# Optimization experiments

Measured on AMD Instinct MI355X. Metric: run time of the kernel, lower is better.

The kernel has to match this reference:

```python
import jax, jax.numpy as jnp
import numpy as np

HEADS = 8
DIM_HEAD = 64
WINDOW = 512
SCALE = DIM_HEAD ** -0.5


def setup_inputs() -> dict:
    key = jax.random.key(0)
    k1, k2, k3 = jax.random.split(key, 3)
    b, dim, n = 2, 256, 32768
    hidden = HEADS * DIM_HEAD  # 512
    x = jax.random.normal(k1, (b, dim, n), dtype=jnp.float32)
    # Conv1d(dim, hidden*3, 1, bias=False) weight -> [3*hidden, dim]
    w_qkv = jax.random.normal(k2, (3 * hidden, dim), dtype=jnp.float32) * (dim ** -0.5)
    # Conv1d(hidden, dim, 1) weight/bias
    w_out = jax.random.normal(k3, (dim, hidden), dtype=jnp.float32) * (hidden ** -0.5)
    b_out = jnp.zeros((dim,), dtype=jnp.float32)
    return {"x": x, "w_qkv": w_qkv, "w_out": w_out, "b_out": b_out}


def reference(x, w_qkv, w_out, b_out):
    b, c, n = x.shape
    h, d, w = HEADS, DIM_HEAD, WINDOW
    nw = n // w  # n chosen divisible by window size
    # 1x1 conv == channel matmul
    qkv = jnp.einsum('oc,bcn->bon', w_qkv, x)  # [b, 3*h*d, n]
    q, k, v = jnp.split(qkv, 3, axis=1)
    # [b, h, d, nw, w]
    def to_windows(t):
        return t.reshape(b, h, d, nw, w)
    q = to_windows(q) * SCALE
    k = to_windows(k)
    v = to_windows(v)
    # non-overlapping local windows: block-diagonal attention
    sim = jnp.einsum('bhdni,bhdnj->bhnij', q, k)        # [b,h,nw,w,w]
    attn = jax.nn.softmax(sim, axis=-1)
    out = jnp.einsum('bhnij,bhdnj->bhdni', attn, v)      # [b,h,d,nw,w]
    out = out.reshape(b, h * d, n)
    return jnp.einsum('oc,bcn->bon', w_out, out) + b_out[None, :, None]
```

## Files before the change

kernel.cpp:

```cpp
#include <hip/hip_runtime.h>
#include <stdint.h>
#include <stddef.h>


typedef _Float16 f16;
typedef _Float16 half8 __attribute__((ext_vector_type(8)));
typedef float f32x4 __attribute__((ext_vector_type(4)));

#define NSEQ 32768
#define NTOT 65536
#define WIN  512

__device__ __forceinline__ void async_copy16(const f16* g, f16* l) {
  __builtin_amdgcn_global_load_lds(
      (const __attribute__((address_space(1))) void*)g,
      (__attribute__((address_space(3))) void*)l, 16, 0, 0);
}

__device__ __forceinline__ int packrtz(float a, float b) {
  typedef __fp16 fp16v2 __attribute__((ext_vector_type(2)));
  fp16v2 h = __builtin_amdgcn_cvt_pkrtz(a, b);
  return __builtin_bit_cast(int, h);
}

__global__ __launch_bounds__(256) void convert_w(
    const float* __restrict__ wqkv, const float* __restrict__ wout,
    f16* __restrict__ wqh, f16* __restrict__ woh) {
  int idx = blockIdx.x * 256 + threadIdx.x;
  if (idx < 1536 * 256) {
    float v = wqkv[idx];
    if (idx < 512 * 256) v *= 0.18033688011112042f;
    wqh[idx] = (f16)v;
  } else {
    int j = idx - 1536 * 256;
    if (j < 256 * 512) woh[j] = (f16)wout[j];
  }
}

__global__ __launch_bounds__(256) void transpose_x(
    const float* __restrict__ x, f16* __restrict__ xT) {
  __shared__ alignas(16) float tile[32][33];
  const int tx = threadIdx.x & 31, ty = threadIdx.x >> 5;
  const int bx = blockIdx.x, by = blockIdx.y;
  const float* xb = x + (size_t)blockIdx.z * 256 * NSEQ;
  f16* xTb = xT + (size_t)blockIdx.z * NSEQ * 256;
#pragma unroll
  for (int r = 0; r < 4; ++r) {
    int c = by * 32 + ty + r * 8;
    int n = bx * 32 + tx;
    tile[ty + r * 8][tx] = xb[(size_t)c * NSEQ + n];
  }
  __syncthreads();
#pragma unroll
  for (int r = 0; r < 4; ++r) {
    int n = bx * 32 + ty + r * 8;
    int c = by * 32 + tx;
    xTb[(size_t)n * 256 + c] = (f16)tile[tx][ty + r * 8];
  }
}

template <int MODE>
__global__ __launch_bounds__(256) void gemm_k(
    const f16* __restrict__ A, const f16* __restrict__ Bm,
    void* __restrict__ outp, const float* __restrict__ bias, int K,
    int bstride, int ostride) {
  __shared__ alignas(16) f16 As[8192];
  __shared__ alignas(16) f16 Bs[8192];
  const int tid = threadIdx.x;
  const int lane = tid & 63, wid = tid >> 6;
  const int quad = lane >> 4, lid = lane & 15;
  const int row0 = blockIdx.y * 128, col0 = blockIdx.x * 128;
  const int wm = (wid >> 1) * 64, wn = (wid & 1) * 64;

  f32x4 acc[4][4];
  const f32x4 zero = {0.f, 0.f, 0.f, 0.f};
#pragma unroll
  for (int i = 0; i < 4; ++i)
#pragma unroll
    for (int j = 0; j < 4; ++j) acc[i][j] = zero;

  const int kIters = K >> 6;
  for (int kt = 0; kt < kIters; ++kt) {
    __syncthreads();
    const int k0 = kt * 64;
#pragma unroll
    for (int rd = 0; rd < 4; ++rd) {
      int slot = rd * 256 + tid;
      int r = slot & 127, kc = slot >> 7;
      async_copy16(A + (size_t)(row0 + r) * K + k0 + kc * 8, As + slot * 8);
      async_copy16(Bm + (size_t)(col0 + r) * bstride + k0 + kc * 8,
                   Bs + slot * 8);
    }
    __syncthreads();

    half8 af[2][4], bf[2][4];
#pragma unroll
    for (int ks = 0; ks < 2; ++ks) {
#pragma unroll
      for (int mi = 0; mi < 4; ++mi)
        af[ks][mi] = *(const half8*)(As + ((ks * 4 + quad) * 128 + wm +
                                           mi * 16 + lid) * 8);
#pragma unroll
      for (int ni = 0; ni < 4; ++ni)
        bf[ks][ni] = *(const half8*)(Bs + ((ks * 4 + quad) * 128 + wn +
                                           ni * 16 + lid) * 8);
    }
#pragma unroll
    for (int ks = 0; ks < 2; ++ks)
#pragma unroll
      for (int mi = 0; mi < 4; ++mi)
#pragma unroll
        for (int ni = 0; ni < 4; ++ni)
          acc[mi][ni] = __builtin_amdgcn_mfma_f32_16x16x32_f16(
              af[ks][mi], bf[ks][ni], acc[mi][ni], 0, 0, 0);
  }

#pragma unroll
  for (int mi = 0; mi < 4; ++mi) {
#pragma unroll
    for (int r = 0; r < 4; ++r) {
      int grow = row0 + wm + mi * 16 + quad * 4 + r;
#pragma unroll
      for (int ni = 0; ni < 4; ++ni) {
        int gcol = col0 + wn + ni * 16 + lid;
        float v = acc[mi][ni][r];
        if (MODE == 2) {
          ((float*)outp)[(size_t)(gcol >> 15) * (256u * 32768u) +
                         (size_t)grow * 32768 + (gcol & 32767)] =
              v + bias[grow];
        } else {
          ((f16*)outp)[(size_t)grow * ostride + gcol] = (f16)v;
        }
      }
    }
  }
}

__global__ __launch_bounds__(512, 2) void attn_k(
    const f16* __restrict__ qk, const f16* __restrict__ vws,
    f16* __restrict__ ows) {
  __shared__ alignas(16) f16 smem[16384];

  const int tid = threadIdx.x;
  const int lane = tid & 63, wid = tid >> 6;
  const int quad = lane >> 4, lid = lane & 15;
  const int win = blockIdx.x;
  const int h = blockIdx.y;
  const size_t nbase = (size_t)blockIdx.z * NSEQ + (size_t)win * WIN;
  const int iw0 = wid * 64;

  half8 aq[4][2];
#pragma unroll
  for (int ig = 0; ig < 4; ++ig)
#pragma unroll
    for (int ks = 0; ks < 2; ++ks)
      aq[ig][ks] = *(const half8*)(qk + (nbase + iw0 + ig * 16 + lid) * 1024 +
                                   h * 64 + ks * 32 + quad * 8);

  f32x4 OT[4][4];
  const f32x4 zero = {0.f, 0.f, 0.f, 0.f};
#pragma unroll
  for (int di = 0; di < 4; ++di)
#pragma unroll
    for (int ig = 0; ig < 4; ++ig) OT[di][ig] = zero;
  float l_run[4] = {0.f, 0.f, 0.f, 0.f};

  const int sa = tid & 63, sc = tid >> 6;
  const int psa = (sa & 32) | ((sa & 12) << 1) | ((sa >> 2) & 4) | (sa & 3);

  async_copy16(qk + (nbase + psa) * 1024 + 512 + h * 64 + sc * 8,
               smem + tid * 8);
  async_copy16(vws + (size_t)(h * 64 + sa) * NTOT + nbase + sc * 8,
               smem + 4096 + tid * 8);

  int p = 0;
  for (int jt = 0; jt < 8; ++jt) {
    __syncthreads();
    if (jt < 7) {
      const int j0n = (jt + 1) * 64;
      f16* Kb = smem + (1 - p) * 8192;
      async_copy16(qk + (nbase + j0n + psa) * 1024 + 512 + h * 64 + sc * 8,
                   Kb + tid * 8);
      async_copy16(vws + (size_t)(h * 64 + sa) * NTOT + nbase + j0n + sc * 8,
                   Kb + 4096 + tid * 8);
    }
    const f16* Ks = smem + p * 8192;
    const f16* Vs = smem + p * 8192 + 4096;

    f32x4 sT[4][4];
#pragma unroll
    for (int jg = 0; jg < 4; ++jg)
#pragma unroll
      for (int ig = 0; ig < 4; ++ig) sT[jg][ig] = zero;
#pragma unroll
    for (int ks = 0; ks < 2; ++ks)
#pragma unroll
      for (int jg = 0; jg < 4; ++jg) {
        half8 bk =
            *(const half8*)(Ks + ((ks * 4 + quad) * 64 + jg * 16 + lid) * 8);
#pragma unroll
        for (int ig = 0; ig < 4; ++ig)
          sT[jg][ig] = __builtin_amdgcn_mfma_f32_16x16x32_f16(
              bk, aq[ig][ks], sT[jg][ig], 0, 0, 0);
      }

    int pk[4][4][2];
#pragma unroll
    for (int jg = 0; jg < 4; ++jg)
#pragma unroll
      for (int ig = 0; ig < 4; ++ig) {
        float e0 = __builtin_amdgcn_exp2f(sT[jg][ig][0]);
        float e1 = __builtin_amdgcn_exp2f(sT[jg][ig][1]);
        float e2 = __builtin_amdgcn_exp2f(sT[jg][ig][2]);
        float e3 = __builtin_amdgcn_exp2f(sT[jg][ig][3]);
        l_run[ig] += (e0 + e1) + (e2 + e3);
        pk[jg][ig][0] = packrtz(e0, e1);
        pk[jg][ig][1] = packrtz(e2, e3);
      }

#pragma unroll
    for (int ks2 = 0; ks2 < 2; ++ks2) {
      const int ta = ks2 * 2, tb = ta + 1;
      half8 pt[4];
#pragma unroll
      for (int ig = 0; ig < 4; ++ig) {
        union {
          int i[4];
          half8 h;
        } u;
        u.i[0] = pk[ta][ig][0];
        u.i[1] = pk[ta][ig][1];
        u.i[2] = pk[tb][ig][0];
        u.i[3] = pk[tb][ig][1];
        pt[ig] = u.h;
      }
#pragma unroll
      for (int di = 0; di < 4; ++di) {
        half8 av =
            *(const half8*)(Vs + ((ks2 * 4 + quad) * 64 + di * 16 + lid) * 8);
#pragma unroll
        for (int ig = 0; ig < 4; ++ig)
          OT[di][ig] = __builtin_amdgcn_mfma_f32_16x16x32_f16(
              av, pt[ig], OT[di][ig], 0, 0, 0);
      }
    }
    p ^= 1;
  }

#pragma unroll
  for (int ig = 0; ig < 4; ++ig) {
    l_run[ig] += __shfl_xor(l_run[ig], 16, 64);
    l_run[ig] += __shfl_xor(l_run[ig], 32, 64);
  }

#pragma unroll
  for (int ig = 0; ig < 4; ++ig) {
    float inv = 1.0f / l_run[ig];
    size_t rowb = (nbase + iw0 + ig * 16 + lid) * 1024 + h * 64;
#pragma unroll
    for (int di = 0; di < 4; ++di) {
      int2 o;
      o.x = packrtz(OT[di][ig][0] * inv, OT[di][ig][1] * inv);
      o.y = packrtz(OT[di][ig][2] * inv, OT[di][ig][3] * inv);
      *(int2*)(ows + rowb + di * 16 + quad * 4) = o;
    }
  }
}

extern "C" void kernel_launch(void* const* d_in, const int* in_sizes, int n_in,
                              void* d_out, int out_size, void* d_ws,
                              size_t ws_size, hipStream_t stream) {
  const float* x = (const float*)d_in[0];
  const float* w_qkv = (const float*)d_in[1];
  const float* w_out = (const float*)d_in[2];
  const float* b_out = (const float*)d_in[3];

  char* ws = (char*)d_ws;
  f16* qkw = (f16*)(ws);
  f16* vw = (f16*)(ws + 134217728);
  f16* xT = (f16*)(ws + 201326592);
  f16* wqh = (f16*)(ws + 234881024);
  f16* woh = (f16*)(ws + 235667456);

  convert_w<<<2048, 256, 0, stream>>>(w_qkv, w_out, wqh, woh);
  transpose_x<<<dim3(1024, 8, 2), 256, 0, stream>>>(x, xT);
  gemm_k<0><<<dim3(8, 512), 256, 0, stream>>>(xT, wqh, qkw, nullptr, 256, 256,
                                              1024);
  gemm_k<0><<<dim3(512, 4), 256, 0, stream>>>(wqh + 1024 * 256, xT, vw,
                                              nullptr, 256, 256, NTOT);
  attn_k<<<dim3(64, 8, 2), 512, 0, stream>>>(qkw, vw, qkw);
  gemm_k<2><<<dim3(512, 2), 256, 0, stream>>>(woh, qkw, d_out, b_out, 512,
                                              1024, 0);
}
```

Baseline: 409.3 us.

## Double-buffer GEMM LDS tiles, swizzle QK GEMM blocks, pack transpose stores

The projection GEMM now keeps two LDS buffers and issues async loads for the next K tile before computing the current one, aiming to overlap global-to-LDS transfer with MFMA work. The QK projection GEMM remaps block indices so that blocks sharing an A row-panel run close together, for cache reuse. The x transpose writes pairs of f16 values as 32-bit stores instead of scalar 16-bit stores. The larger LDS footprint may lower occupancy.

```diff
diff --git a/kernel.cpp b/kernel.cpp
--- a/kernel.cpp
+++ b/kernel.cpp
@@ -51,25 +51,43 @@
     tile[ty + r * 8][tx] = xb[(size_t)c * NSEQ + n];
   }
   __syncthreads();
-#pragma unroll
-  for (int r = 0; r < 4; ++r) {
-    int n = bx * 32 + ty + r * 8;
-    int c = by * 32 + tx;
-    xTb[(size_t)n * 256 + c] = (f16)tile[tx][ty + r * 8];
-  }
-}
-
-template <int MODE>
+  const int tx16 = threadIdx.x & 15, ty16 = threadIdx.x >> 4;
+#pragma unroll
+  for (int r = 0; r < 2; ++r) {
+    int n = bx * 32 + ty16 + r * 16;
+    int c = by * 32 + tx16 * 2;
+    union {
+      f16 h[2];
+      int i;
+    } u;
+    u.h[0] = (f16)tile[tx16 * 2][ty16 + r * 16];
+    u.h[1] = (f16)tile[tx16 * 2 + 1][ty16 + r * 16];
+    *(int*)(xTb + (size_t)n * 256 + c) = u.i;
+  }
+}
+
+template <int MODE, int SWZ>
 __global__ __launch_bounds__(256) void gemm_k(
     const f16* __restrict__ A, const f16* __restrict__ Bm,
     void* __restrict__ outp, const float* __restrict__ bias, int K,
     int bstride, int ostride) {
-  __shared__ alignas(16) f16 As[8192];
-  __shared__ alignas(16) f16 Bs[8192];
+  __shared__ alignas(16) f16 As[2][8192];
+  __shared__ alignas(16) f16 Bs[2][8192];
   const int tid = threadIdx.x;
   const int lane = tid & 63, wid = tid >> 6;
   const int quad = lane >> 4, lid = lane & 15;
-  const int row0 = blockIdx.y * 128, col0 = blockIdx.x * 128;
+
+  int colb, rowb;
+  if (SWZ) {
+    int lin = blockIdx.y * 8 + blockIdx.x;
+    int x = lin & 7, s = lin >> 3;
+    colb = s & 7;
+    rowb = x * 64 + (s >> 3);
+  } else {
+    colb = blockIdx.x;
+    rowb = blockIdx.y;
+  }
+  const int row0 = rowb * 128, col0 = colb * 128;
   const int wm = (wid >> 1) * 64, wn = (wid & 1) * 64;
 
   f32x4 acc[4][4];
@@ -80,30 +98,37 @@
     for (int j = 0; j < 4; ++j) acc[i][j] = zero;
 
   const int kIters = K >> 6;
-  for (int kt = 0; kt < kIters; ++kt) {
-    __syncthreads();
+
+  auto stage = [&](int kt, int buf) {
     const int k0 = kt * 64;
 #pragma unroll
     for (int rd = 0; rd < 4; ++rd) {
       int slot = rd * 256 + tid;
       int r = slot & 127, kc = slot >> 7;
-      async_copy16(A + (size_t)(row0 + r) * K + k0 + kc * 8, As + slot * 8);
+      async_copy16(A + (size_t)(row0 + r) * K + k0 + kc * 8,
+                   &As[buf][slot * 8]);
       async_copy16(Bm + (size_t)(col0 + r) * bstride + k0 + kc * 8,
-                   Bs + slot * 8);
-    }
+                   &Bs[buf][slot * 8]);
+    }
+  };
+
+  stage(0, 0);
+  int p = 0;
+  for (int kt = 0; kt < kIters; ++kt) {
     __syncthreads();
+    if (kt + 1 < kIters) stage(kt + 1, p ^ 1);
 
     half8 af[2][4], bf[2][4];
 #pragma unroll
     for (int ks = 0; ks < 2; ++ks) {
 #pragma unroll
       for (int mi = 0; mi < 4; ++mi)
-        af[ks][mi] = *(const half8*)(As + ((ks * 4 + quad) * 128 + wm +
-                                           mi * 16 + lid) * 8);
+        af[ks][mi] = *(const half8*)(&As[p][((ks * 4 + quad) * 128 + wm +
+                                             mi * 16 + lid) * 8]);
 #pragma unroll
       for (int ni = 0; ni < 4; ++ni)
-        bf[ks][ni] = *(const half8*)(Bs + ((ks * 4 + quad) * 128 + wn +
-                                           ni * 16 + lid) * 8);
+        bf[ks][ni] = *(const half8*)(&Bs[p][((ks * 4 + quad) * 128 + wn +
+                                             ni * 16 + lid) * 8]);
     }
 #pragma unroll
     for (int ks = 0; ks < 2; ++ks)
@@ -113,6 +138,7 @@
         for (int ni = 0; ni < 4; ++ni)
           acc[mi][ni] = __builtin_amdgcn_mfma_f32_16x16x32_f16(
               af[ks][mi], bf[ks][ni], acc[mi][ni], 0, 0, 0);
+    p ^= 1;
   }
 
 #pragma unroll
@@ -284,11 +310,11 @@
 
   convert_w<<<2048, 256, 0, stream>>>(w_qkv, w_out, wqh, woh);
   transpose_x<<<dim3(1024, 8, 2), 256, 0, stream>>>(x, xT);
-  gemm_k<0><<<dim3(8, 512), 256, 0, stream>>>(xT, wqh, qkw, nullptr, 256, 256,
-                                              1024);
-  gemm_k<0><<<dim3(512, 4), 256, 0, stream>>>(wqh + 1024 * 256, xT, vw,
-                                              nullptr, 256, 256, NTOT);
+  gemm_k<0, 1><<<dim3(8, 512), 256, 0, stream>>>(xT, wqh, qkw, nullptr, 256,
+                                                 256, 1024);
+  gemm_k<0, 0><<<dim3(512, 4), 256, 0, stream>>>(wqh + 1024 * 256, xT, vw,
+                                                 nullptr, 256, 256, NTOT);
   attn_k<<<dim3(64, 8, 2), 512, 0, stream>>>(qkw, vw, qkw);
-  gemm_k<2><<<dim3(512, 2), 256, 0, stream>>>(woh, qkw, d_out, b_out, 512,
-                                              1024, 0);
-}
+  gemm_k<2, 0><<<dim3(512, 2), 256, 0, stream>>>(woh, qkw, d_out, b_out, 512,
+                                                 1024, 0);
+}
```

Measured after the change: 393.1 us. 4.0% less time.
